# Performance work log

Hardware: AMD Instinct MI355X
Metric: run time of the kernel (lower is better)

Reference implementation:

```python
import jax, jax.numpy as jnp
import numpy as np
from jax import lax

NUM_SPLIT = 16
DCT = 7
# top16 frequency indices (first 16 of the top lists)
MAPPER_X = np.array([0, 0, 6, 0, 0, 1, 1, 4, 5, 1, 3, 0, 0, 0, 3, 2], dtype=np.int32)
MAPPER_Y = np.array([0, 1, 0, 5, 2, 0, 2, 0, 0, 6, 0, 4, 6, 3, 5, 2], dtype=np.int32)


def _dct_table():
    pos = np.arange(DCT)
    freq = np.arange(DCT)[:, None]
    d = np.cos(np.pi * freq * (pos + 0.5) / DCT) / np.sqrt(DCT)
    d[1:] *= np.sqrt(2.0)
    return d.astype(np.float32)  # (7, 7): [freq, pos]


def _gconv(x, w, b, groups):
    y = lax.conv_general_dilated(x, w, (2, 2), 'VALID',
                                 dimension_numbers=('NCHW', 'OIHW', 'NCHW'),
                                 feature_group_count=groups)
    return y + b[None, :, None, None]


def setup_inputs() -> dict:
    key = jax.random.key(0)
    ks = jax.random.split(key, 7)
    n, c, h, w = 32, 512, 56, 56
    r = 16
    return {
        'x': jax.random.normal(ks[0], (n, c, h, w), jnp.float32),
        'conv1_w': jax.random.normal(ks[1], (NUM_SPLIT, c // NUM_SPLIT, 3, 3), jnp.float32) * 0.05,
        'conv1_b': jax.random.normal(ks[2], (NUM_SPLIT,), jnp.float32) * 0.05,
        'conv2_w': jax.random.normal(ks[3], (NUM_SPLIT, 1, 3, 3), jnp.float32) * 0.3,
        'conv2_b': jax.random.normal(ks[4], (NUM_SPLIT,), jnp.float32) * 0.3,
        'w1': jax.random.normal(ks[5], (c // r, c), jnp.float32) * 0.05,
        'w2': jax.random.normal(ks[6], (c, c // r), jnp.float32) * 0.2,
    }


def reference(x, conv1_w, conv1_b, conv2_w, conv2_b, w1, w2):
    n, c, h, w = x.shape
    c_part = c // NUM_SPLIT
    D = jnp.asarray(_dct_table(), x.dtype)
    mx = jnp.asarray(MAPPER_X)
    my = jnp.asarray(MAPPER_Y)

    # adaptive_avg_pool2d to 7x7 (h,w divisible by 7 -> exact block mean)
    xp = x.reshape(n, c, DCT, h // DCT, DCT, w // DCT).mean(axis=(3, 5))

    # filters_predicted: grouped conv 7x7 -> 3x3 -> 1x1
    a1 = jax.nn.hard_sigmoid(_gconv(xp, conv1_w, conv1_b, NUM_SPLIT))
    v = _gconv(a1, conv2_w, conv2_b, NUM_SPLIT).reshape(n, NUM_SPLIT)
    # adaptive_avg_pool1d(1 -> 16) repeats v; matmul with ones(16,1) sums -> v * 16
    pred = jnp.clip(v * NUM_SPLIT, 0.0, NUM_SPLIT - 1.1)

    left = pred.astype(jnp.int32)   # (n, 16)
    frac = pred - left
    right = left + 1

    def dct_weights(idx):  # idx (n,16) -> per-split 7x7 DCT filters (n,16,7,7)
        fx = D[mx[idx]]  # (n,16,7)
        fy = D[my[idx]]
        return fx[..., :, None] * fy[..., None, :]

    xp_s = xp.reshape(n, NUM_SPLIT, c_part, DCT, DCT)
    res_l = jnp.einsum('nskhw,nshw->nsk', xp_s, dct_weights(left)) * (1.0 - frac)[:, :, None]
    res_r = jnp.einsum('nskhw,nshw->nsk', xp_s, dct_weights(right)) * frac[:, :, None]
    s = (res_l + res_r).reshape(n, c)

    hmid = jax.nn.hard_sigmoid(s @ w1.T)
    cw = jax.nn.sigmoid(hmid @ w2.T)  # (n, c)
    return x * cw[:, :, None, None]
```

## Files before the change

### kernel.cpp

```cpp
#include <hip/hip_runtime.h>

#define N_   32
#define C_   512
#define H_   56
#define W_   56
#define S_   16
#define CP_  32
#define HW_  (H_*W_)
#define TOT_ ((size_t)N_*C_*HW_)

__constant__ int d_mx[16] = {0,0,6,0,0,1,1,4,5,1,3,0,0,0,3,2};
__constant__ int d_my[16] = {0,1,0,5,2,0,2,0,0,6,0,4,6,3,5,2};

__global__ void __launch_bounds__(64) pool_kernel(const float* __restrict__ x,
                                                  float* __restrict__ xp) {
    int plane = blockIdx.x;
    int t = threadIdx.x;
    if (t >= 49) return;
    int oi = t / 7, oj = t % 7;
    const float* p = x + (size_t)plane * HW_ + (oi * 8) * W_ + oj * 8;
    float sum = 0.f;
#pragma unroll
    for (int r = 0; r < 8; ++r) {
        float4 a = *reinterpret_cast<const float4*>(p + r * W_);
        float4 b = *reinterpret_cast<const float4*>(p + r * W_ + 4);
        sum += a.x + a.y + a.z + a.w + b.x + b.y + b.z + b.w;
    }
    xp[(size_t)plane * 49 + t] = sum * (1.0f / 64.0f);
}

__global__ void __launch_bounds__(256) head_kernel(
        const float* __restrict__ xp,
        const float* __restrict__ c1w, const float* __restrict__ c1b,
        const float* __restrict__ c2w, const float* __restrict__ c2b,
        const float* __restrict__ w1,  const float* __restrict__ w2,
        float* __restrict__ cwout) {
    __shared__ float sD[7][7];
    __shared__ float a1[S_ * 9];
    __shared__ float wcomb[S_ * 49];
    __shared__ float svec[C_];
    __shared__ float hmid[32];
    __shared__ float sfrac[S_];
    __shared__ int   sleft[S_];

    int n = blockIdx.x, t = threadIdx.x;
    const float* xpn = xp + (size_t)n * C_ * 49;

    if (t < 49) {
        int f = t / 7, p = t % 7;
        float v = cosf(3.14159265358979323846f * f * (p + 0.5f) / 7.0f) * 0.3779644730092272f;
        if (f >= 1) v *= 1.4142135623730951f;
        sD[f][p] = v;
    }
    __syncthreads();

    if (t < S_ * 9) {
        int s = t / 9, o = t - s * 9, oi = o / 3, oj = o - oi * 3;
        float acc = c1b[s];
        const float* xb = xpn + s * CP_ * 49;
        const float* wb = c1w + s * CP_ * 9;
        for (int ic = 0; ic < CP_; ++ic) {
#pragma unroll
            for (int ki = 0; ki < 3; ++ki)
#pragma unroll
                for (int kj = 0; kj < 3; ++kj)
                    acc += xb[ic * 49 + (oi * 2 + ki) * 7 + (oj * 2 + kj)]
                         * wb[ic * 9 + ki * 3 + kj];
        }
        a1[t] = fminf(fmaxf(acc + 3.f, 0.f), 6.f) * (1.f / 6.f);
    }
    __syncthreads();

    if (t < S_) {
        float acc = c2b[t];
#pragma unroll
        for (int k = 0; k < 9; ++k) acc += a1[t * 9 + k] * c2w[t * 9 + k];
        float pred = fminf(fmaxf(acc * 16.f, 0.f), 14.9f);
        int l = (int)pred;
        sleft[t] = l;
        sfrac[t] = pred - (float)l;
    }
    __syncthreads();

    for (int i = t; i < S_ * 49; i += 256) {
        int s = i / 49, p = i - s * 49, hh = p / 7, ww = p - hh * 7;
        int l = sleft[s], r = l + 1;
        float fr = sfrac[s];
        wcomb[i] = (1.f - fr) * sD[d_mx[l]][hh] * sD[d_my[l]][ww]
                 +        fr  * sD[d_mx[r]][hh] * sD[d_my[r]][ww];
    }
    __syncthreads();

    for (int ch = t; ch < C_; ch += 256) {
        const float* xb = xpn + ch * 49;
        const float* wb = &wcomb[(ch >> 5) * 49];
        float acc = 0.f;
#pragma unroll
        for (int p = 0; p < 49; ++p) acc += xb[p] * wb[p];
        svec[ch] = acc;
    }
    __syncthreads();

    if (t < 32) {
        float acc = 0.f;
        const float* wr = w1 + t * C_;
        for (int k = 0; k < C_; ++k) acc += svec[k] * wr[k];
        hmid[t] = fminf(fmaxf(acc + 3.f, 0.f), 6.f) * (1.f / 6.f);
    }
    __syncthreads();

    for (int ch = t; ch < C_; ch += 256) {
        float acc = 0.f;
        const float* wr = w2 + ch * 32;
#pragma unroll
        for (int j = 0; j < 32; ++j) acc += hmid[j] * wr[j];
        cwout[n * C_ + ch] = 1.f / (1.f + expf(-acc));
    }
}

__global__ void __launch_bounds__(256) scale_kernel(const float* __restrict__ x,
                                                    const float* __restrict__ cw,
                                                    float* __restrict__ out) {
    unsigned int i = blockIdx.x * 256u + threadIdx.x;
    unsigned int plane = i / 784u;
    float wsc = cw[plane];
    float4 u = reinterpret_cast<const float4*>(x)[i];
    u.x *= wsc; u.y *= wsc; u.z *= wsc; u.w *= wsc;
    reinterpret_cast<float4*>(out)[i] = u;
}

extern "C" void kernel_launch(void* const* d_in, const int* in_sizes, int n_in,
                              void* d_out, int out_size, void* d_ws, size_t ws_size,
                              hipStream_t stream) {
    const float* x   = (const float*)d_in[0];
    const float* c1w = (const float*)d_in[1];
    const float* c1b = (const float*)d_in[2];
    const float* c2w = (const float*)d_in[3];
    const float* c2b = (const float*)d_in[4];
    const float* w1  = (const float*)d_in[5];
    const float* w2  = (const float*)d_in[6];
    float* out = (float*)d_out;

    float* xp    = (float*)d_ws;
    float* cwbuf = xp + (size_t)N_ * C_ * 49;

    pool_kernel<<<N_ * C_, 64, 0, stream>>>(x, xp);
    head_kernel<<<N_, 256, 0, stream>>>(xp, c1w, c1b, c2w, c2b, w1, w2, cwbuf);
    scale_kernel<<<(unsigned)(TOT_ / 4 / 256), 256, 0, stream>>>(x, cwbuf, out);
}
```

Before: 407.6 us.

## Stage pool planes and head inputs through LDS with coalesced loads and split reductions

The pool kernel now runs 256 threads per plane. Each block copies the whole 56x56 plane into shared memory with coalesced float4 loads, then reduces each 8x8 bin in four parts. The head kernel stages the per-sample pooled activations into shared memory in two chunks for the grouped conv. It spreads the w1 matvec across all 256 threads with vectorized partial sums and vectorizes the w2 dot products. The aim is to replace strided, poorly coalesced global reads and serial single-thread loops with wider loads and more parallelism, at the cost of a larger LDS footprint and extra barriers.

```diff
diff --git a/kernel.cpp b/kernel.cpp
--- a/kernel.cpp
+++ b/kernel.cpp
@@ -12,21 +12,32 @@
 __constant__ int d_mx[16] = {0,0,6,0,0,1,1,4,5,1,3,0,0,0,3,2};
 __constant__ int d_my[16] = {0,1,0,5,2,0,2,0,0,6,0,4,6,3,5,2};
 
-__global__ void __launch_bounds__(64) pool_kernel(const float* __restrict__ x,
-                                                  float* __restrict__ xp) {
+__global__ void __launch_bounds__(256) pool_kernel(const float* __restrict__ x,
+                                                   float* __restrict__ xp) {
+    __shared__ float tile[HW_];
+    __shared__ float part[49 * 4];
     int plane = blockIdx.x;
     int t = threadIdx.x;
-    if (t >= 49) return;
-    int oi = t / 7, oj = t % 7;
-    const float* p = x + (size_t)plane * HW_ + (oi * 8) * W_ + oj * 8;
-    float sum = 0.f;
+    const float4* src = reinterpret_cast<const float4*>(x + (size_t)plane * HW_);
+    for (int i = t; i < HW_ / 4; i += 256)
+        *reinterpret_cast<float4*>(&tile[i * 4]) = src[i];
+    __syncthreads();
+    if (t < 196) {
+        int bin = t >> 2, q = t & 3;
+        int oi = bin / 7, oj = bin % 7;
+        const float* rp = &tile[(oi * 8 + q * 2) * W_ + oj * 8];
+        float s = 0.f;
 #pragma unroll
-    for (int r = 0; r < 8; ++r) {
-        float4 a = *reinterpret_cast<const float4*>(p + r * W_);
-        float4 b = *reinterpret_cast<const float4*>(p + r * W_ + 4);
-        sum += a.x + a.y + a.z + a.w + b.x + b.y + b.z + b.w;
+        for (int rr = 0; rr < 2; ++rr)
+#pragma unroll
+            for (int cc = 0; cc < 8; ++cc) s += rp[rr * W_ + cc];
+        part[t] = s;
     }
-    xp[(size_t)plane * 49 + t] = sum * (1.0f / 64.0f);
+    __syncthreads();
+    if (t < 49) {
+        float s = part[t * 4] + part[t * 4 + 1] + part[t * 4 + 2] + part[t * 4 + 3];
+        xp[(size_t)plane * 49 + t] = s * (1.0f / 64.0f);
+    }
 }
 
 __global__ void __launch_bounds__(256) head_kernel(
@@ -35,10 +46,12 @@
         const float* __restrict__ c2w, const float* __restrict__ c2b,
         const float* __restrict__ w1,  const float* __restrict__ w2,
         float* __restrict__ cwout) {
+    __shared__ float tile[8 * CP_ * 49];
     __shared__ float sD[7][7];
     __shared__ float a1[S_ * 9];
     __shared__ float wcomb[S_ * 49];
     __shared__ float svec[C_];
+    __shared__ float hpart[256];
     __shared__ float hmid[32];
     __shared__ float sfrac[S_];
     __shared__ int   sleft[S_];
@@ -52,22 +65,29 @@
         if (f >= 1) v *= 1.4142135623730951f;
         sD[f][p] = v;
     }
-    __syncthreads();
 
-    if (t < S_ * 9) {
-        int s = t / 9, o = t - s * 9, oi = o / 3, oj = o - oi * 3;
-        float acc = c1b[s];
-        const float* xb = xpn + s * CP_ * 49;
-        const float* wb = c1w + s * CP_ * 9;
-        for (int ic = 0; ic < CP_; ++ic) {
+    for (int chunk = 0; chunk < 2; ++chunk) {
+        __syncthreads();
+        const float4* src = reinterpret_cast<const float4*>(xpn + chunk * 8 * CP_ * 49);
+        for (int i = t; i < 8 * CP_ * 49 / 4; i += 256)
+            *reinterpret_cast<float4*>(&tile[i * 4]) = src[i];
+        __syncthreads();
+        if (t < 72) {
+            int sl = t / 9, o = t - sl * 9, oi = o / 3, oj = o - oi * 3;
+            int s = chunk * 8 + sl;
+            float acc = c1b[s];
+            const float* xb = &tile[sl * CP_ * 49];
+            const float* wb = c1w + s * CP_ * 9;
+            for (int ic = 0; ic < CP_; ++ic) {
 #pragma unroll
-            for (int ki = 0; ki < 3; ++ki)
+                for (int ki = 0; ki < 3; ++ki)
 #pragma unroll
-                for (int kj = 0; kj < 3; ++kj)
-                    acc += xb[ic * 49 + (oi * 2 + ki) * 7 + (oj * 2 + kj)]
-                         * wb[ic * 9 + ki * 3 + kj];
+                    for (int kj = 0; kj < 3; ++kj)
+                        acc += xb[ic * 49 + (oi * 2 + ki) * 7 + (oj * 2 + kj)]
+                             * wb[ic * 9 + ki * 3 + kj];
+            }
+            a1[s * 9 + o] = fminf(fmaxf(acc + 3.f, 0.f), 6.f) * (1.f / 6.f);
         }
-        a1[t] = fminf(fmaxf(acc + 3.f, 0.f), 6.f) * (1.f / 6.f);
     }
     __syncthreads();
 
@@ -92,7 +112,8 @@
     __syncthreads();
 
     for (int ch = t; ch < C_; ch += 256) {
-        const float* xb = xpn + ch * 49;
+        const float* xb = (ch < 256) ? (xpn + ch * 49)
+                                     : (&tile[(ch - 256) * 49]);
         const float* wb = &wcomb[(ch >> 5) * 49];
         float acc = 0.f;
 #pragma unroll
@@ -101,19 +122,36 @@
     }
     __syncthreads();
 
+    {
+        int o = t >> 3, g = t & 7;
+        const float4* wv = reinterpret_cast<const float4*>(w1 + o * C_ + g * 64);
+        const float4* sv = reinterpret_cast<const float4*>(&svec[g * 64]);
+        float acc = 0.f;
+#pragma unroll
+        for (int j = 0; j < 16; ++j) {
+            float4 a = sv[j], b = wv[j];
+            acc += a.x * b.x + a.y * b.y + a.z * b.z + a.w * b.w;
+        }
+        hpart[t] = acc;
+    }
+    __syncthreads();
     if (t < 32) {
         float acc = 0.f;
-        const float* wr = w1 + t * C_;
-        for (int k = 0; k < C_; ++k) acc += svec[k] * wr[k];
+#pragma unroll
+        for (int g = 0; g < 8; ++g) acc += hpart[t * 8 + g];
         hmid[t] = fminf(fmaxf(acc + 3.f, 0.f), 6.f) * (1.f / 6.f);
     }
     __syncthreads();
 
     for (int ch = t; ch < C_; ch += 256) {
+        const float4* wr = reinterpret_cast<const float4*>(w2 + ch * 32);
         float acc = 0.f;
-        const float* wr = w2 + ch * 32;
 #pragma unroll
-        for (int j = 0; j < 32; ++j) acc += hmid[j] * wr[j];
+        for (int j = 0; j < 8; ++j) {
+            float4 b = wr[j];
+            const float4 h = reinterpret_cast<const float4*>(hmid)[j];
+            acc += h.x * b.x + h.y * b.y + h.z * b.z + h.w * b.w;
+        }
         cwout[n * C_ + ch] = 1.f / (1.f + expf(-acc));
     }
 }
@@ -144,7 +182,7 @@
     float* xp    = (float*)d_ws;
     float* cwbuf = xp + (size_t)N_ * C_ * 49;
 
-    pool_kernel<<<N_ * C_, 64, 0, stream>>>(x, xp);
+    pool_kernel<<<N_ * C_, 256, 0, stream>>>(x, xp);
     head_kernel<<<N_, 256, 0, stream>>>(xp, c1w, c1b, c2w, c2b, w1, w2, cwbuf);
     scale_kernel<<<(unsigned)(TOT_ / 4 / 256), 256, 0, stream>>>(x, cwbuf, out);
 }
```

Measured after the change: 401.6 us. Within noise of the previous version (-1.5%).
